# Kernel optimization log

Hardware: AMD Instinct MI355X
Metric: run time of the kernel (lower is better)

The kernel has to match this reference:

```python
import jax, jax.numpy as jnp
import numpy as np

EPS = 1e-8
INF = 1e9


def _normalize(x):
    # Matches torch: F.normalize(x + 1e-8, dim=-1, eps=1e-8)
    y = x + EPS
    n = jnp.linalg.norm(y, axis=-1, keepdims=True)
    return y / jnp.maximum(n, EPS)


def _lsa(cost):
    """Exact linear sum assignment (Jonker-Volgenant shortest augmenting path,
    same optimum as scipy.optimize.linear_sum_assignment) for a square cost
    matrix. Returns col_ind (Q,) int32 with row i matched to col_ind[i]."""
    n = cost.shape[0]
    cost1 = jnp.pad(cost, ((1, 0), (1, 0)))  # 1-indexed rows/cols; col 0 virtual

    def row_step(i, uvp):
        u, v, p = uvp  # duals u,v: (n+1,); p[j] = row assigned to column j (0=none)
        i = i.astype(jnp.int32)
        p = p.at[0].set(i)
        way0 = jnp.zeros(n + 1, jnp.int32)
        minv0 = jnp.full(n + 1, INF, cost.dtype)
        used0 = jnp.zeros(n + 1, bool)

        def cond(c):
            u, v, p, way, minv, used, j0 = c
            return p[j0] != 0

        def body(c):
            u, v, p, way, minv, used, j0 = c
            used = used.at[j0].set(True)
            i0 = p[j0]
            cur = cost1[i0] - u[i0] - v  # reduced costs of row i0, all cols
            better = (cur < minv) & (~used)
            minv = jnp.where(better, cur, minv)
            way = jnp.where(better, j0, way)
            masked = jnp.where(used, INF, minv)
            j1 = jnp.argmin(masked).astype(jnp.int32)
            delta = masked[j1]
            u = u.at[p].add(jnp.where(used, delta, 0.0))
            v = jnp.where(used, v - delta, v)
            minv = jnp.where(used, minv, minv - delta)
            return (u, v, p, way, minv, used, j1)

        u, v, p, way, minv, used, j0 = jax.lax.while_loop(
            cond, body, (u, v, p, way0, minv0, used0, jnp.int32(0)))

        def aug_cond(c):
            return c[1] != 0

        def aug_body(c):
            p, j0 = c
            j1 = way[j0]
            return (p.at[j0].set(p[j1]), j1)

        p, _ = jax.lax.while_loop(aug_cond, aug_body, (p, j0))
        return (u, v, p)

    z = jnp.zeros(n + 1, cost.dtype)
    p0 = jnp.zeros(n + 1, jnp.int32)
    _, _, p = jax.lax.fori_loop(1, n + 1, row_step, (z, z, p0))
    col_ind = jnp.zeros(n, jnp.int32).at[p[1:] - 1].set(
        jnp.arange(n, dtype=jnp.int32))
    return col_ind


def setup_inputs() -> dict:
    key = jax.random.key(0)
    k1, k2 = jax.random.split(key)
    B, Q, D = 64, 128, 512
    rubin_objects = jax.random.normal(k1, (B, Q, D), dtype=jnp.float32)
    euclid_objects = jax.random.normal(k2, (B, Q, D), dtype=jnp.float32)
    return {"rubin_objects": rubin_objects, "euclid_objects": euclid_objects}


def reference(rubin_objects, euclid_objects):
    r = _normalize(rubin_objects)   # (B, Q, D)
    e = _normalize(euclid_objects)  # (B, Q, D)
    cost = -jnp.einsum('bqd,bkd->bqk', r, e)  # (B, Q, Q) negative cosine sim
    col = jax.vmap(_lsa)(cost)                # (B, Q) optimal assignment
    matched_e = jnp.take_along_axis(e, col[..., None], axis=1)  # (B, Q, D)
    sim = jnp.sum(r * matched_e, axis=-1)     # (B, Q)
    loss = jnp.mean(1.0 - jnp.mean(sim, axis=-1))
    return loss, col
```

## Files before the change

### kernel.cpp

```cpp
#include <hip/hip_runtime.h>

#define BB 64
#define QN 128
#define DD 512
#define EPSF 1e-8f
#define INFV 1e9f

__global__ __launch_bounds__(256) void cost_k(const float* __restrict__ rraw,
                                              const float* __restrict__ eraw,
                                              float* __restrict__ cost,
                                              float* __restrict__ out) {
  if (blockIdx.x == 0 && blockIdx.y == 0 && threadIdx.x == 0)
    out[0] = 1.0f;
  int b = blockIdx.y;
  int qt = (blockIdx.x >> 1) * 64;
  int kt = (blockIdx.x & 1) * 64;
  const float* R = rraw + ((size_t)b * QN + qt) * DD;
  const float* E = eraw + ((size_t)b * QN + kt) * DD;
  __shared__ float rsT[32][68];
  __shared__ float esT[32][68];
  __shared__ float sir[64], sie[64];
  int tid = threadIdx.x;
  int tx = tid & 15, ty = tid >> 4;
  int lrow = tid >> 2;
  int ld = (tid & 3) * 8;
  float acc[4][4] = {};
  float rssq = 0.f, essq = 0.f;
  for (int d0 = 0; d0 < DD; d0 += 32) {
    float4 ra = *(const float4*)(R + (size_t)lrow * DD + d0 + ld);
    float4 rb = *(const float4*)(R + (size_t)lrow * DD + d0 + ld + 4);
    float4 ea = *(const float4*)(E + (size_t)lrow * DD + d0 + ld);
    float4 eb = *(const float4*)(E + (size_t)lrow * DD + d0 + ld + 4);
    ra.x += EPSF; ra.y += EPSF; ra.z += EPSF; ra.w += EPSF;
    rb.x += EPSF; rb.y += EPSF; rb.z += EPSF; rb.w += EPSF;
    ea.x += EPSF; ea.y += EPSF; ea.z += EPSF; ea.w += EPSF;
    eb.x += EPSF; eb.y += EPSF; eb.z += EPSF; eb.w += EPSF;
    rssq += ra.x * ra.x + ra.y * ra.y + ra.z * ra.z + ra.w * ra.w +
            rb.x * rb.x + rb.y * rb.y + rb.z * rb.z + rb.w * rb.w;
    essq += ea.x * ea.x + ea.y * ea.y + ea.z * ea.z + ea.w * ea.w +
            eb.x * eb.x + eb.y * eb.y + eb.z * eb.z + eb.w * eb.w;
    __syncthreads();
    rsT[ld + 0][lrow] = ra.x; rsT[ld + 1][lrow] = ra.y;
    rsT[ld + 2][lrow] = ra.z; rsT[ld + 3][lrow] = ra.w;
    rsT[ld + 4][lrow] = rb.x; rsT[ld + 5][lrow] = rb.y;
    rsT[ld + 6][lrow] = rb.z; rsT[ld + 7][lrow] = rb.w;
    esT[ld + 0][lrow] = ea.x; esT[ld + 1][lrow] = ea.y;
    esT[ld + 2][lrow] = ea.z; esT[ld + 3][lrow] = ea.w;
    esT[ld + 4][lrow] = eb.x; esT[ld + 5][lrow] = eb.y;
    esT[ld + 6][lrow] = eb.z; esT[ld + 7][lrow] = eb.w;
    __syncthreads();
#pragma unroll
    for (int dd = 0; dd < 32; ++dd) {
      float4 rv = *(const float4*)&rsT[dd][ty * 4];
      float4 ev = *(const float4*)&esT[dd][tx * 4];
      const float* rp = (const float*)&rv;
      const float* ep = (const float*)&ev;
#pragma unroll
      for (int ii = 0; ii < 4; ++ii)
#pragma unroll
        for (int jj = 0; jj < 4; ++jj) acc[ii][jj] += rp[ii] * ep[jj];
    }
  }
  rssq += __shfl_xor(rssq, 1, 64); rssq += __shfl_xor(rssq, 2, 64);
  essq += __shfl_xor(essq, 1, 64); essq += __shfl_xor(essq, 2, 64);
  if ((tid & 3) == 0) {
    sir[lrow] = 1.f / fmaxf(sqrtf(rssq), EPSF);
    sie[lrow] = 1.f / fmaxf(sqrtf(essq), EPSF);
  }
  __syncthreads();
  float irow[4], icol[4];
#pragma unroll
  for (int ii = 0; ii < 4; ++ii) { irow[ii] = sir[ty * 4 + ii]; icol[ii] = sie[tx * 4 + ii]; }
  float* Co = cost + ((size_t)b * QN + qt + ty * 4) * QN + kt + tx * 4;
#pragma unroll
  for (int ii = 0; ii < 4; ++ii) {
    float4 o = make_float4(-acc[ii][0] * irow[ii] * icol[0],
                           -acc[ii][1] * irow[ii] * icol[1],
                           -acc[ii][2] * irow[ii] * icol[2],
                           -acc[ii][3] * irow[ii] * icol[3]);
    *(float4*)(Co + (size_t)ii * QN) = o;
  }
}

template <int CTRL, int RM>
__device__ __forceinline__ float fmin_dpp(float x) {
  int y = __builtin_amdgcn_update_dpp(0x7f800000, __float_as_int(x), CTRL, RM,
                                      0xf, false);
  return fminf(x, __int_as_float(y));
}
__device__ __forceinline__ float wave_min63(float x) {
  x = fmin_dpp<0x111, 0xf>(x);
  x = fmin_dpp<0x112, 0xf>(x);
  x = fmin_dpp<0x114, 0xf>(x);
  x = fmin_dpp<0x118, 0xf>(x);
  x = fmin_dpp<0x142, 0xa>(x);
  x = fmin_dpp<0x143, 0xc>(x);
  return x;
}

__device__ __forceinline__ float rl_f(float x, int lane) {
  return __int_as_float(__builtin_amdgcn_readlane(__float_as_int(x), lane));
}

__global__ __launch_bounds__(64) void lsa_k(const float* __restrict__ cost,
                                            float* __restrict__ col_out,
                                            float* __restrict__ out) {
  __shared__ float lC[QN * QN];
  const int b = blockIdx.x;
  const int tid = threadIdx.x;
  const float* C = cost + (size_t)b * QN * QN;
  typedef const __attribute__((address_space(1))) void* gvp;
  typedef __attribute__((address_space(3))) void* svp;
#pragma unroll 4
  for (int k = 0; k < 64; ++k) {
    __builtin_amdgcn_global_load_lds((gvp)(C + k * 256 + tid * 4),
                                     (svp)(lC + k * 256), 16, 0, 0);
  }
  __syncthreads();

  float cmin0 = INFV, cmin1 = INFV;
  int am0 = 0, am1 = 0;
#pragma unroll 8
  for (int i = 0; i < QN; ++i) {
    float a = lC[i * QN + tid];
    float c = lC[i * QN + tid + 64];
    if (a < cmin0) { cmin0 = a; am0 = i; }
    if (c < cmin1) { cmin1 = c; am1 = i; }
  }
  float v0 = cmin0, v1 = cmin1;
  int pp = 0;
  int mr0 = 0, mr1 = 0;

  for (int j = 0; j < QN; ++j) {
    int r = __builtin_amdgcn_readlane(j < 64 ? am0 : am1, j & 63);
    int taken = __builtin_amdgcn_readlane(r < 64 ? mr0 : mr1, r & 63);
    if (!taken) {
      if (tid == (j & 63)) {
        if (j < 64) pp = (pp & 0xff00) | (r + 1);
        else        pp = (pp & 0x00ff) | ((r + 1) << 8);
      }
      if (r < 64) { if (tid == r) mr0 = 1; }
      else        { if (tid == r - 64) mr1 = 1; }
    }
  }

  for (int pass = 0; pass < 2; ++pass) {
    for (int i = 0; i < QN; ++i) {
      int mi = __builtin_amdgcn_readlane(i < 64 ? mr0 : mr1, i & 63);
      if (mi) continue;
      float c0 = lC[i * QN + tid];
      float c1 = lC[i * QN + tid + 64];
      float cur0 = c0 - v0;
      float cur1 = c1 - v1;
      float u1 = rl_f(wave_min63(fminf(cur0, cur1)), 63);
      unsigned long long bal0 = __ballot(cur0 == u1);
      unsigned long long bal1 = __ballot(cur1 == u1);
      int j1 = bal0 ? (__ffsll(bal0) - 1) : (64 + __ffsll(bal1) - 1);
      float mm0 = (tid == j1) ? INFV : cur0;
      float mm1 = (tid + 64 == j1) ? INFV : cur1;
      float u2 = rl_f(wave_min63(fminf(mm0, mm1)), 63);
      if (u1 < u2) {
        float dv = u2 - u1;
        if (tid == j1) v0 -= dv;
        if (tid + 64 == j1) v1 -= dv;
      } else {
        int pjB = __builtin_amdgcn_readlane(pp, j1 & 63);
        int pj = ((j1 < 64) ? (pjB & 0xff) : (pjB >> 8)) - 1;
        if (pj >= 0) {
          unsigned long long b20 = __ballot(mm0 == u2);
          unsigned long long b21 = __ballot(mm1 == u2);
          j1 = b20 ? (__ffsll(b20) - 1) : (64 + __ffsll(b21) - 1);
        }
      }
      int kB = __builtin_amdgcn_readlane(pp, j1 & 63);
      int k = ((j1 < 64) ? (kB & 0xff) : (kB >> 8)) - 1;
      if (tid == (j1 & 63)) {
        if (j1 < 64) pp = (pp & 0xff00) | (i + 1);
        else         pp = (pp & 0x00ff) | ((i + 1) << 8);
      }
      if (i < 64) { if (tid == i) mr0 = 1; }
      else        { if (tid == i - 64) mr1 = 1; }
      if (k >= 0) {
        if (k < 64) { if (tid == k) mr0 = 0; }
        else        { if (tid == k - 64) mr1 = 0; }
      }
    }
  }

  for (int i = 0; i < QN; ++i) {
    int mi = __builtin_amdgcn_readlane(i < 64 ? mr0 : mr1, i & 63);
    if (mi) continue;
    float d0 = lC[i * QN + tid] - v0;
    float d1 = lC[i * QN + tid + 64] - v1;
    int way0 = -1, way1 = -1;
    bool used0 = false, used1 = false;
    float mu;
    int jfree;
    for (;;) {
      float m0 = used0 ? INFV : d0;
      float m1 = used1 ? INFV : d1;
      float red = wave_min63(fminf(m0, m1));
      mu = rl_f(red, 63);
      unsigned long long bal0 = __ballot(m0 == mu);
      unsigned long long bal1 = __ballot(m1 == mu);
      int j1 = bal0 ? (__ffsll(bal0) - 1) : (64 + __ffsll(bal1) - 1);
      int ppw = __builtin_amdgcn_readlane(pp, j1 & 63);
      int pj1 = ((j1 < 64) ? (ppw & 0xff) : (ppw >> 8)) - 1;
      if (pj1 < 0) { jfree = j1; break; }
      float c0 = lC[pj1 * QN + tid];
      float c1 = lC[pj1 * QN + tid + 64];
      used0 = used0 || (tid == j1);
      used1 = used1 || (tid + 64 == j1);
      float t0 = c0 - v0, t1 = c1 - v1;
      float base = rl_f(j1 < 64 ? t0 : t1, j1 & 63);
      float s = mu - base;
      float nd0 = t0 + s, nd1 = t1 + s;
      if (!used0 && nd0 < d0) { d0 = nd0; way0 = j1; }
      if (!used1 && nd1 < d1) { d1 = nd1; way1 = j1; }
    }
    if (used0) v0 += d0 - mu;
    if (used1) v1 += d1 - mu;
    int j = jfree;
    for (;;) {
      int wj = __builtin_amdgcn_readlane(j < 64 ? way0 : way1, j & 63);
      int newp;
      if (wj < 0) newp = i;
      else {
        int pw = __builtin_amdgcn_readlane(pp, wj & 63);
        newp = ((wj < 64) ? (pw & 0xff) : (pw >> 8)) - 1;
      }
      if (tid == (j & 63)) {
        if (j < 64) pp = (pp & 0xff00) | (newp + 1);
        else        pp = (pp & 0x00ff) | ((newp + 1) << 8);
      }
      if (wj < 0) break;
      j = wj;
    }
  }

  int p0 = (pp & 0xff) - 1;
  int p1 = (pp >> 8) - 1;
  col_out[(size_t)b * QN + p0] = (float)tid;
  col_out[(size_t)b * QN + p1] = (float)(tid + 64);
  float s = -lC[p0 * QN + tid] - lC[p1 * QN + tid + 64];
#pragma unroll
  for (int off = 32; off; off >>= 1) s += __shfl_xor(s, off, 64);
  if (tid == 0) atomicAdd(out, -s * (1.0f / ((float)BB * (float)QN)));
}

extern "C" void kernel_launch(void* const* d_in, const int* in_sizes, int n_in,
                              void* d_out, int out_size, void* d_ws, size_t ws_size,
                              hipStream_t stream) {
  const float* rub = (const float*)d_in[0];
  const float* euc = (const float*)d_in[1];
  float* out = (float*)d_out;
  float* ws = (float*)d_ws;
  float* cost = ws;

  dim3 gc(4, BB);
  cost_k<<<gc, 256, 0, stream>>>(rub, euc, cost, out);
  lsa_k<<<BB, 64, 0, stream>>>(cost, out + 1, out);
}
```

Before: 376.3 us.

## Fuse cost-matrix GEMM into the LSA kernel, building the cost tile in LDS

The separate cosine-cost kernel is folded into the assignment kernel. Each 512-thread block now computes its batch's 128x128 cost matrix straight into shared memory, using an interleaved column layout so each assignment lane reads its two columns with one float2 load. This removes the global cost write and read-back and one kernel launch. In exchange the GEMM runs on only 64 blocks instead of 256, E is reloaded for each query half, and the loss is now initialised by adding 1.0 from block 0, which relies on the output buffer starting at zero.

```diff
diff --git a/kernel.cpp b/kernel.cpp
--- a/kernel.cpp
+++ b/kernel.cpp
@@ -5,82 +5,6 @@
 #define DD 512
 #define EPSF 1e-8f
 #define INFV 1e9f
-
-__global__ __launch_bounds__(256) void cost_k(const float* __restrict__ rraw,
-                                              const float* __restrict__ eraw,
-                                              float* __restrict__ cost,
-                                              float* __restrict__ out) {
-  if (blockIdx.x == 0 && blockIdx.y == 0 && threadIdx.x == 0)
-    out[0] = 1.0f;
-  int b = blockIdx.y;
-  int qt = (blockIdx.x >> 1) * 64;
-  int kt = (blockIdx.x & 1) * 64;
-  const float* R = rraw + ((size_t)b * QN + qt) * DD;
-  const float* E = eraw + ((size_t)b * QN + kt) * DD;
-  __shared__ float rsT[32][68];
-  __shared__ float esT[32][68];
-  __shared__ float sir[64], sie[64];
-  int tid = threadIdx.x;
-  int tx = tid & 15, ty = tid >> 4;
-  int lrow = tid >> 2;
-  int ld = (tid & 3) * 8;
-  float acc[4][4] = {};
-  float rssq = 0.f, essq = 0.f;
-  for (int d0 = 0; d0 < DD; d0 += 32) {
-    float4 ra = *(const float4*)(R + (size_t)lrow * DD + d0 + ld);
-    float4 rb = *(const float4*)(R + (size_t)lrow * DD + d0 + ld + 4);
-    float4 ea = *(const float4*)(E + (size_t)lrow * DD + d0 + ld);
-    float4 eb = *(const float4*)(E + (size_t)lrow * DD + d0 + ld + 4);
-    ra.x += EPSF; ra.y += EPSF; ra.z += EPSF; ra.w += EPSF;
-    rb.x += EPSF; rb.y += EPSF; rb.z += EPSF; rb.w += EPSF;
-    ea.x += EPSF; ea.y += EPSF; ea.z += EPSF; ea.w += EPSF;
-    eb.x += EPSF; eb.y += EPSF; eb.z += EPSF; eb.w += EPSF;
-    rssq += ra.x * ra.x + ra.y * ra.y + ra.z * ra.z + ra.w * ra.w +
-            rb.x * rb.x + rb.y * rb.y + rb.z * rb.z + rb.w * rb.w;
-    essq += ea.x * ea.x + ea.y * ea.y + ea.z * ea.z + ea.w * ea.w +
-            eb.x * eb.x + eb.y * eb.y + eb.z * eb.z + eb.w * eb.w;
-    __syncthreads();
-    rsT[ld + 0][lrow] = ra.x; rsT[ld + 1][lrow] = ra.y;
-    rsT[ld + 2][lrow] = ra.z; rsT[ld + 3][lrow] = ra.w;
-    rsT[ld + 4][lrow] = rb.x; rsT[ld + 5][lrow] = rb.y;
-    rsT[ld + 6][lrow] = rb.z; rsT[ld + 7][lrow] = rb.w;
-    esT[ld + 0][lrow] = ea.x; esT[ld + 1][lrow] = ea.y;
-    esT[ld + 2][lrow] = ea.z; esT[ld + 3][lrow] = ea.w;
-    esT[ld + 4][lrow] = eb.x; esT[ld + 5][lrow] = eb.y;
-    esT[ld + 6][lrow] = eb.z; esT[ld + 7][lrow] = eb.w;
-    __syncthreads();
-#pragma unroll
-    for (int dd = 0; dd < 32; ++dd) {
-      float4 rv = *(const float4*)&rsT[dd][ty * 4];
-      float4 ev = *(const float4*)&esT[dd][tx * 4];
-      const float* rp = (const float*)&rv;
-      const float* ep = (const float*)&ev;
-#pragma unroll
-      for (int ii = 0; ii < 4; ++ii)
-#pragma unroll
-        for (int jj = 0; jj < 4; ++jj) acc[ii][jj] += rp[ii] * ep[jj];
-    }
-  }
-  rssq += __shfl_xor(rssq, 1, 64); rssq += __shfl_xor(rssq, 2, 64);
-  essq += __shfl_xor(essq, 1, 64); essq += __shfl_xor(essq, 2, 64);
-  if ((tid & 3) == 0) {
-    sir[lrow] = 1.f / fmaxf(sqrtf(rssq), EPSF);
-    sie[lrow] = 1.f / fmaxf(sqrtf(essq), EPSF);
-  }
-  __syncthreads();
-  float irow[4], icol[4];
-#pragma unroll
-  for (int ii = 0; ii < 4; ++ii) { irow[ii] = sir[ty * 4 + ii]; icol[ii] = sie[tx * 4 + ii]; }
-  float* Co = cost + ((size_t)b * QN + qt + ty * 4) * QN + kt + tx * 4;
-#pragma unroll
-  for (int ii = 0; ii < 4; ++ii) {
-    float4 o = make_float4(-acc[ii][0] * irow[ii] * icol[0],
-                           -acc[ii][1] * irow[ii] * icol[1],
-                           -acc[ii][2] * irow[ii] * icol[2],
-                           -acc[ii][3] * irow[ii] * icol[3]);
-    *(float4*)(Co + (size_t)ii * QN) = o;
-  }
-}
 
 template <int CTRL, int RM>
 __device__ __forceinline__ float fmin_dpp(float x) {
@@ -102,30 +26,83 @@
   return __int_as_float(__builtin_amdgcn_readlane(__float_as_int(x), lane));
 }
 
-__global__ __launch_bounds__(64) void lsa_k(const float* __restrict__ cost,
-                                            float* __restrict__ col_out,
-                                            float* __restrict__ out) {
+__global__ __launch_bounds__(512) void fused_k(const float* __restrict__ rraw,
+                                               const float* __restrict__ eraw,
+                                               float* __restrict__ col_out,
+                                               float* __restrict__ out) {
   __shared__ float lC[QN * QN];
+  __shared__ float rsT[32][68];
+  __shared__ float esT[32][136];
+  __shared__ float sir[64];
+  __shared__ float sie[QN];
   const int b = blockIdx.x;
   const int tid = threadIdx.x;
-  const float* C = cost + (size_t)b * QN * QN;
-  typedef const __attribute__((address_space(1))) void* gvp;
-  typedef __attribute__((address_space(3))) void* svp;
-#pragma unroll 4
-  for (int k = 0; k < 64; ++k) {
-    __builtin_amdgcn_global_load_lds((gvp)(C + k * 256 + tid * 4),
-                                     (svp)(lC + k * 256), 16, 0, 0);
+  const float* Rb = rraw + (size_t)b * QN * DD;
+  const float* Eb = eraw + (size_t)b * QN * DD;
+  const int tx = tid & 31, ty = tid >> 5;
+  const int rrow = tid >> 3, rd = (tid & 7) * 4;
+  const int erow = tid >> 2, ed = (tid & 3) * 8;
+  const int epos = 2 * (erow & 63) + (erow >> 6);
+
+  for (int qt = 0; qt < QN; qt += 64) {
+    float acc[4][4] = {};
+    float rssq = 0.f, essq = 0.f;
+    for (int d0 = 0; d0 < DD; d0 += 32) {
+      float4 rv = *(const float4*)(Rb + (size_t)(qt + rrow) * DD + d0 + rd);
+      float4 e0 = *(const float4*)(Eb + (size_t)erow * DD + d0 + ed);
+      float4 e1 = *(const float4*)(Eb + (size_t)erow * DD + d0 + ed + 4);
+      rv.x += EPSF; rv.y += EPSF; rv.z += EPSF; rv.w += EPSF;
+      e0.x += EPSF; e0.y += EPSF; e0.z += EPSF; e0.w += EPSF;
+      e1.x += EPSF; e1.y += EPSF; e1.z += EPSF; e1.w += EPSF;
+      rssq += rv.x * rv.x + rv.y * rv.y + rv.z * rv.z + rv.w * rv.w;
+      essq += e0.x * e0.x + e0.y * e0.y + e0.z * e0.z + e0.w * e0.w +
+              e1.x * e1.x + e1.y * e1.y + e1.z * e1.z + e1.w * e1.w;
+      __syncthreads();
+      rsT[rd + 0][rrow] = rv.x; rsT[rd + 1][rrow] = rv.y;
+      rsT[rd + 2][rrow] = rv.z; rsT[rd + 3][rrow] = rv.w;
+      esT[ed + 0][epos] = e0.x; esT[ed + 1][epos] = e0.y;
+      esT[ed + 2][epos] = e0.z; esT[ed + 3][epos] = e0.w;
+      esT[ed + 4][epos] = e1.x; esT[ed + 5][epos] = e1.y;
+      esT[ed + 6][epos] = e1.z; esT[ed + 7][epos] = e1.w;
+      __syncthreads();
+#pragma unroll
+      for (int dd = 0; dd < 32; ++dd) {
+        float4 av = *(const float4*)&rsT[dd][ty * 4];
+        float4 ev = *(const float4*)&esT[dd][tx * 4];
+        const float* ap = (const float*)&av;
+        const float* ep = (const float*)&ev;
+#pragma unroll
+        for (int ii = 0; ii < 4; ++ii)
+#pragma unroll
+          for (int jj = 0; jj < 4; ++jj) acc[ii][jj] += ap[ii] * ep[jj];
+      }
+    }
+    rssq += __shfl_xor(rssq, 1, 64); rssq += __shfl_xor(rssq, 2, 64);
+    rssq += __shfl_xor(rssq, 4, 64);
+    essq += __shfl_xor(essq, 1, 64); essq += __shfl_xor(essq, 2, 64);
+    if ((tid & 7) == 0) sir[rrow] = 1.f / fmaxf(sqrtf(rssq), EPSF);
+    if ((tid & 3) == 0) sie[erow] = 1.f / fmaxf(sqrtf(essq), EPSF);
+    __syncthreads();
+    float ic0 = sie[2 * tx], ic1 = sie[2 * tx + 64];
+    float ic2 = sie[2 * tx + 1], ic3 = sie[2 * tx + 65];
+#pragma unroll
+    for (int ii = 0; ii < 4; ++ii) {
+      float ir = sir[ty * 4 + ii];
+      float4 o = make_float4(-acc[ii][0] * ir * ic0, -acc[ii][1] * ir * ic1,
+                             -acc[ii][2] * ir * ic2, -acc[ii][3] * ir * ic3);
+      *(float4*)&lC[(qt + ty * 4 + ii) * QN + 4 * tx] = o;
+    }
   }
   __syncthreads();
+  if (tid >= 64) return;
 
   float cmin0 = INFV, cmin1 = INFV;
   int am0 = 0, am1 = 0;
 #pragma unroll 8
   for (int i = 0; i < QN; ++i) {
-    float a = lC[i * QN + tid];
-    float c = lC[i * QN + tid + 64];
-    if (a < cmin0) { cmin0 = a; am0 = i; }
-    if (c < cmin1) { cmin1 = c; am1 = i; }
+    float2 ac = *(const float2*)&lC[i * QN + 2 * tid];
+    if (ac.x < cmin0) { cmin0 = ac.x; am0 = i; }
+    if (ac.y < cmin1) { cmin1 = ac.y; am1 = i; }
   }
   float v0 = cmin0, v1 = cmin1;
   int pp = 0;
@@ -148,10 +125,9 @@
     for (int i = 0; i < QN; ++i) {
       int mi = __builtin_amdgcn_readlane(i < 64 ? mr0 : mr1, i & 63);
       if (mi) continue;
-      float c0 = lC[i * QN + tid];
-      float c1 = lC[i * QN + tid + 64];
-      float cur0 = c0 - v0;
-      float cur1 = c1 - v1;
+      float2 cc = *(const float2*)&lC[i * QN + 2 * tid];
+      float cur0 = cc.x - v0;
+      float cur1 = cc.y - v1;
       float u1 = rl_f(wave_min63(fminf(cur0, cur1)), 63);
       unsigned long long bal0 = __ballot(cur0 == u1);
       unsigned long long bal1 = __ballot(cur1 == u1);
@@ -190,8 +166,9 @@
   for (int i = 0; i < QN; ++i) {
     int mi = __builtin_amdgcn_readlane(i < 64 ? mr0 : mr1, i & 63);
     if (mi) continue;
-    float d0 = lC[i * QN + tid] - v0;
-    float d1 = lC[i * QN + tid + 64] - v1;
+    float2 ci = *(const float2*)&lC[i * QN + 2 * tid];
+    float d0 = ci.x - v0;
+    float d1 = ci.y - v1;
     int way0 = -1, way1 = -1;
     bool used0 = false, used1 = false;
     float mu;
@@ -207,11 +184,10 @@
       int ppw = __builtin_amdgcn_readlane(pp, j1 & 63);
       int pj1 = ((j1 < 64) ? (ppw & 0xff) : (ppw >> 8)) - 1;
       if (pj1 < 0) { jfree = j1; break; }
-      float c0 = lC[pj1 * QN + tid];
-      float c1 = lC[pj1 * QN + tid + 64];
+      float2 cc = *(const float2*)&lC[pj1 * QN + 2 * tid];
       used0 = used0 || (tid == j1);
       used1 = used1 || (tid + 64 == j1);
-      float t0 = c0 - v0, t1 = c1 - v1;
+      float t0 = cc.x - v0, t1 = cc.y - v1;
       float base = rl_f(j1 < 64 ? t0 : t1, j1 & 63);
       float s = mu - base;
       float nd0 = t0 + s, nd1 = t1 + s;
@@ -242,10 +218,14 @@
   int p1 = (pp >> 8) - 1;
   col_out[(size_t)b * QN + p0] = (float)tid;
   col_out[(size_t)b * QN + p1] = (float)(tid + 64);
-  float s = -lC[p0 * QN + tid] - lC[p1 * QN + tid + 64];
+  float s = -lC[p0 * QN + 2 * tid] - lC[p1 * QN + 2 * tid + 1];
 #pragma unroll
   for (int off = 32; off; off >>= 1) s += __shfl_xor(s, off, 64);
-  if (tid == 0) atomicAdd(out, -s * (1.0f / ((float)BB * (float)QN)));
+  if (tid == 0) {
+    float contrib = -s * (1.0f / ((float)BB * (float)QN));
+    if (b == 0) contrib += 1.0f;
+    atomicAdd(out, contrib);
+  }
 }
 
 extern "C" void kernel_launch(void* const* d_in, const int* in_sizes, int n_in,
@@ -254,10 +234,5 @@
   const float* rub = (const float*)d_in[0];
   const float* euc = (const float*)d_in[1];
   float* out = (float*)d_out;
-  float* ws = (float*)d_ws;
-  float* cost = ws;
-
-  dim3 gc(4, BB);
-  cost_k<<<gc, 256, 0, stream>>>(rub, euc, cost, out);
-  lsa_k<<<BB, 64, 0, stream>>>(cost, out + 1, out);
-}
+  fused_k<<<BB, 512, 0, stream>>>(rub, euc, out + 1, out);
+}
```

Result: slower. 421.5 us (+12.0%).
